# Kernel tuning notes

Measured on AMD Instinct MI355X. Metric: run time of the kernel, lower is better.

Reference implementation:

```python
import jax, jax.numpy as jnp
import numpy as np

B, S, D = 1, 2048, 1024   # batch, seq, hidden_size
I = 2048                  # intermediate_size (mlp1 emits 2*I, SwiGLU halves)
E = 8                     # num_experts
K = 2                     # experts_per_token
LIMIT = 7.0               # swiglu_limit
ALPHA = 1.702             # gpt-oss swiglu alpha
EPS = 1e-5                # RMSNorm eps


def setup_inputs() -> dict:
    key = jax.random.key(0)
    ks = jax.random.split(key, 4)
    s = 0.02
    return {
        "x": jax.random.normal(ks[0], (B, S, D), jnp.float32),
        "norm_scale": jnp.ones((D,), jnp.float32),
        "gate_w": jax.random.normal(ks[1], (D, E), jnp.float32) * s,
        "gate_b": jnp.zeros((E,), jnp.float32),
        "mlp1_w": jax.random.normal(ks[2], (E, D, 2 * I), jnp.float32) * s,
        "mlp1_b": jnp.zeros((E, 2 * I), jnp.float32),
        "mlp2_w": jax.random.normal(ks[3], (E, I, D), jnp.float32) * s,
        "mlp2_b": jnp.zeros((E, D), jnp.float32),
    }


def _swiglu(h):
    # gpt-oss interleaved SwiGLU with clamp limit
    x_glu = jnp.minimum(h[..., ::2], LIMIT)
    x_lin = jnp.clip(h[..., 1::2], -LIMIT, LIMIT)
    return x_glu * jax.nn.sigmoid(ALPHA * x_glu) * (x_lin + 1.0)


def _moe(t, gate_w, gate_b, mlp1_w, mlp1_b, mlp2_w, mlp2_b):
    T = t.shape[0]
    logits = t @ gate_w + gate_b                 # [T, E]
    top_v, top_i = jax.lax.top_k(logits, K)      # [T, K]
    probs = jax.nn.softmax(top_v, axis=-1)       # softmax over selected experts
    # dense routing-weight matrix, zero for unselected experts
    w = jnp.zeros((T, E), t.dtype).at[jnp.arange(T)[:, None], top_i].set(probs)

    def body(acc, ew):
        w1, b1, w2, b2, we = ew                  # per-expert params + weights [T]
        h = _swiglu(t @ w1 + b1)                 # [T, I]
        y = h @ w2 + b2                          # [T, D]
        return acc + we[:, None] * y, None

    acc0 = jnp.zeros((T, t.shape[1]), t.dtype)
    acc, _ = jax.lax.scan(body, acc0, (mlp1_w, mlp1_b, mlp2_w, mlp2_b, w.T))
    return acc


def reference(x, norm_scale, gate_w, gate_b, mlp1_w, mlp1_b, mlp2_w, mlp2_b):
    Bx, Sx, Dx = x.shape
    ms = jnp.mean(x * x, axis=-1, keepdims=True)
    t = (x * jax.lax.rsqrt(ms + EPS) * norm_scale).reshape(Bx * Sx, Dx)
    y = _moe(t, gate_w, gate_b, mlp1_w, mlp1_b, mlp2_w, mlp2_b)
    return x + y.reshape(Bx, Sx, Dx)
```

## Files before the change

### kernel.cpp

```cpp
#include <hip/hip_runtime.h>

typedef unsigned short u16;
typedef __attribute__((ext_vector_type(4))) unsigned short u16x4;
typedef __attribute__((ext_vector_type(8))) unsigned short u16x8;
typedef __attribute__((ext_vector_type(8))) short bf16x8;
typedef __attribute__((ext_vector_type(4))) float f32x4;

#define DEV static __device__ __forceinline__

DEV float bf2f(u16 b){ union{unsigned u; float f;} c; c.u = ((unsigned)b) << 16; return c.f; }
DEV u16 f2bf(float f){ union{float f; unsigned u;} c; c.f = f; unsigned u = c.u; u += 0x7FFF + ((u >> 16) & 1); return (u16)(u >> 16); }

DEV void gload16(const void* g, void* l){
  __builtin_amdgcn_global_load_lds((const __attribute__((address_space(1))) unsigned int*)g,
                                   (__attribute__((address_space(3))) unsigned int*)l, 16, 0, 0);
}

__global__ __launch_bounds__(256) void k_rms(
    const float* __restrict__ x, const float* __restrict__ nsc,
    const float* __restrict__ gw, const float* __restrict__ gb,
    u16* __restrict__ t, int* __restrict__ topi, float* __restrict__ topp)
{
  const int token = blockIdx.x, tid = threadIdx.x;
  const int wv = tid >> 6, lane = tid & 63;
  const float4 xv = *(const float4*)&x[(size_t)token * 1024 + tid * 4];
  float f[4] = {xv.x, xv.y, xv.z, xv.w};
  float ss = f[0]*f[0] + f[1]*f[1] + f[2]*f[2] + f[3]*f[3];
  #pragma unroll
  for (int o = 32; o > 0; o >>= 1) ss += __shfl_down(ss, o, 64);
  __shared__ float red[4];
  __shared__ float s_rs;
  if (lane == 0) red[wv] = ss;
  __syncthreads();
  if (tid == 0) s_rs = rsqrtf((red[0] + red[1] + red[2] + red[3]) * (1.0f / 1024.0f) + 1e-5f);
  __syncthreads();
  const float rs = s_rs;
  const float4 sv = *(const float4*)&nsc[tid * 4];
  const float sc[4] = {sv.x, sv.y, sv.z, sv.w};
  float tf[4]; u16x4 tv;
  #pragma unroll
  for (int j = 0; j < 4; ++j){ tf[j] = f[j] * rs * sc[j]; tv[j] = f2bf(tf[j]); }
  *(u16x4*)&t[(size_t)token * 1024 + tid * 4] = tv;

  float la[8] = {0,0,0,0,0,0,0,0};
  #pragma unroll
  for (int j = 0; j < 4; ++j){
    const int k = tid * 4 + j;
    const float4 g0 = *(const float4*)&gw[k * 8];
    const float4 g1 = *(const float4*)&gw[k * 8 + 4];
    la[0] += tf[j] * g0.x; la[1] += tf[j] * g0.y; la[2] += tf[j] * g0.z; la[3] += tf[j] * g0.w;
    la[4] += tf[j] * g1.x; la[5] += tf[j] * g1.y; la[6] += tf[j] * g1.z; la[7] += tf[j] * g1.w;
  }
  #pragma unroll
  for (int o = 32; o > 0; o >>= 1)
    #pragma unroll
    for (int e = 0; e < 8; ++e) la[e] += __shfl_down(la[e], o, 64);
  __shared__ float lred[4][8];
  if (lane == 0){
    #pragma unroll
    for (int e = 0; e < 8; ++e) lred[wv][e] = la[e];
  }
  __syncthreads();
  if (tid == 0){
    float lg[8];
    #pragma unroll
    for (int e = 0; e < 8; ++e) lg[e] = lred[0][e] + lred[1][e] + lred[2][e] + lred[3][e] + gb[e];
    int i0 = 0;
    for (int e = 1; e < 8; ++e) if (lg[e] > lg[i0]) i0 = e;
    int i1 = -1;
    for (int e = 0; e < 8; ++e) if (e != i0 && (i1 < 0 || lg[e] > lg[i1])) i1 = e;
    const float d = __expf(lg[i1] - lg[i0]);
    const float p0 = 1.0f / (1.0f + d);
    topi[token * 2] = i0; topi[token * 2 + 1] = i1;
    topp[token * 2] = p0; topp[token * 2 + 1] = d * p0;
  }
}

__global__ __launch_bounds__(256) void k_route(
    const int* __restrict__ topi, const float* __restrict__ topp,
    int* __restrict__ cnt, int* __restrict__ offs, int* __restrict__ tok_of,
    float* __restrict__ wt_of, int* __restrict__ slot_of, int* __restrict__ posg)
{
  __shared__ int c[8];
  __shared__ int o[8];
  const int tid = threadIdx.x;
  if (tid < 8) c[tid] = 0;
  __syncthreads();
  for (int a = tid; a < 4096; a += 256){
    int e = topi[a];
    posg[a] = atomicAdd(&c[e], 1);
  }
  __syncthreads();
  if (tid == 0){
    int run = 0;
    for (int e = 0; e < 8; ++e){ o[e] = run; offs[e] = run; cnt[e] = c[e]; run += c[e]; }
  }
  __syncthreads();
  for (int a = tid; a < 4096; a += 256){
    int e = topi[a];
    int s = o[e] + posg[a];
    tok_of[s] = a >> 1;
    wt_of[s] = topp[a];
    slot_of[a] = s;
  }
}

__global__ __launch_bounds__(256) void k_tr(const float* __restrict__ in, u16* __restrict__ outp, int R, int C)
{
  __shared__ __attribute__((aligned(16))) u16 tile[64][72];
  const size_t base = (size_t)blockIdx.z * (size_t)R * (size_t)C;
  const float* src = in + base;
  u16* dst = outp + base;
  const int r0 = blockIdx.y * 64, c0 = blockIdx.x * 64;
  const int tid = threadIdx.x;
  const int lr = tid >> 4;
  const int lc = (tid & 15) * 4;
  #pragma unroll
  for (int i = 0; i < 4; ++i){
    const float4 v = *(const float4*)&src[(size_t)(r0 + lr + i * 16) * C + c0 + lc];
    u16x4 b; b[0] = f2bf(v.x); b[1] = f2bf(v.y); b[2] = f2bf(v.z); b[3] = f2bf(v.w);
    *(u16x4*)&tile[lr + i * 16][lc] = b;
  }
  __syncthreads();
  const int lr2 = tid >> 3;
  const int lc2 = (tid & 7) * 8;
  #pragma unroll
  for (int i = 0; i < 2; ++i){
    const int cc = lr2 + i * 32;
    u16x8 v;
    #pragma unroll
    for (int j = 0; j < 8; ++j) v[j] = tile[lc2 + j][cc];
    *(u16x8*)&dst[(size_t)(c0 + cc) * R + r0 + lc2] = v;
  }
}

__global__ __launch_bounds__(256) void k_gemm1(
    const u16* __restrict__ t, const u16* __restrict__ w1t, const float* __restrict__ b1,
    const int* __restrict__ cnt, const int* __restrict__ offs, const int* __restrict__ tok_of,
    u16* __restrict__ h)
{
  const int e = blockIdx.z;
  const int count = cnt[e];
  const int m0 = blockIdx.y * 128;
  if (m0 >= count) return;
  const int off = offs[e];
  const int n0 = blockIdx.x * 128;

  __shared__ __attribute__((aligned(16))) u16 As[128 * 32];
  __shared__ __attribute__((aligned(16))) u16 Bs[128 * 32];

  const int tid = threadIdx.x, wv = tid >> 6, lane = tid & 63;
  const int srow = wv * 32 + (lane >> 2);
  const int kc = (lane & 3) * 8;

  const u16* aptr[2]; const u16* bptr[2];
  #pragma unroll
  for (int i = 0; i < 2; ++i){
    int r = m0 + srow + i * 16; if (r > count - 1) r = count - 1;
    const int tok = tok_of[off + r];
    aptr[i] = t + (size_t)tok * 1024 + kc;
    bptr[i] = w1t + ((size_t)e * 4096 + n0 + srow + i * 16) * 1024 + kc;
  }
  u16* lA0 = &As[(wv * 32) * 32];      u16* lA1 = &As[(wv * 32 + 16) * 32];
  u16* lB0 = &Bs[(wv * 32) * 32];      u16* lB1 = &Bs[(wv * 32 + 16) * 32];

  const int wm = wv & 1, wn = wv >> 1;
  const int fr = lane & 15, q8 = (lane >> 4) * 8;

  f32x4 acc[4][4];
  #pragma unroll
  for (int a = 0; a < 4; ++a)
    #pragma unroll
    for (int b = 0; b < 4; ++b) acc[a][b] = (f32x4){0.f, 0.f, 0.f, 0.f};

  for (int k0 = 0; k0 < 1024; k0 += 32){
    gload16(aptr[0], lA0); gload16(aptr[1], lA1);
    gload16(bptr[0], lB0); gload16(bptr[1], lB1);
    aptr[0] += 32; aptr[1] += 32; bptr[0] += 32; bptr[1] += 32;
    __syncthreads();
    bf16x8 af[4], bq[4];
    #pragma unroll
    for (int fm = 0; fm < 4; ++fm) af[fm] = *(const bf16x8*)&As[(wm * 64 + fm * 16 + fr) * 32 + q8];
    #pragma unroll
    for (int fn = 0; fn < 4; ++fn) bq[fn] = *(const bf16x8*)&Bs[(wn * 64 + fn * 16 + fr) * 32 + q8];
    #pragma unroll
    for (int fm = 0; fm < 4; ++fm)
      #pragma unroll
      for (int fn = 0; fn < 4; ++fn)
        acc[fm][fn] = __builtin_amdgcn_mfma_f32_16x16x32_bf16(af[fm], bq[fn], acc[fm][fn], 0, 0, 0);
    __syncthreads();
  }

  const int cb = n0 + wn * 64 + fr;
  float b1v[4];
  #pragma unroll
  for (int fn = 0; fn < 4; ++fn) b1v[fn] = b1[e * 4096 + cb + fn * 16];
  const int rq = (lane >> 4) * 4;
  const bool ev = ((lane & 1) == 0);
  #pragma unroll
  for (int fm = 0; fm < 4; ++fm)
    #pragma unroll
    for (int fn = 0; fn < 4; ++fn)
      #pragma unroll
      for (int r = 0; r < 4; ++r){
        const float val = acc[fm][fn][r] + b1v[fn];
        const float oth = __shfl_xor(val, 1, 64);
        if (ev){
          const int row = m0 + wm * 64 + fm * 16 + rq + r;
          if (row < count){
            const float g = fminf(val, 7.0f);
            const float l = fminf(fmaxf(oth, -7.0f), 7.0f);
            const float o = g / (1.0f + __expf(-1.702f * g)) * (l + 1.0f);
            h[(size_t)(off + row) * 2048 + ((cb + fn * 16) >> 1)] = f2bf(o);
          }
        }
      }
}

__global__ __launch_bounds__(256) void k_gemm2(
    const u16* __restrict__ h, const u16* __restrict__ w2t, const float* __restrict__ b2,
    const int* __restrict__ cnt, const int* __restrict__ offs, const float* __restrict__ wt_of,
    u16* __restrict__ ys)
{
  const int e = blockIdx.z;
  const int count = cnt[e];
  const int m0 = blockIdx.y * 64;
  if (m0 >= count) return;
  const int off = offs[e];
  const int n0 = blockIdx.x * 64;

  __shared__ __attribute__((aligned(16))) u16 As[64 * 32];
  __shared__ __attribute__((aligned(16))) u16 Bs[64 * 32];

  const int tid = threadIdx.x, wv = tid >> 6, lane = tid & 63;
  const int srow = wv * 16 + (lane >> 2);
  const int kc = (lane & 3) * 8;
  int r = m0 + srow; if (r > count - 1) r = count - 1;
  const u16* aptr = h + (size_t)(off + r) * 2048 + kc;
  const u16* bptr = w2t + ((size_t)e * 1024 + n0 + srow) * 2048 + kc;
  u16* lA = &As[(wv * 16) * 32];
  u16* lB = &Bs[(wv * 16) * 32];

  const int wm = wv & 1, wn = wv >> 1;
  const int fr = lane & 15, q8 = (lane >> 4) * 8;

  f32x4 acc[2][2];
  #pragma unroll
  for (int a = 0; a < 2; ++a)
    #pragma unroll
    for (int b = 0; b < 2; ++b) acc[a][b] = (f32x4){0.f, 0.f, 0.f, 0.f};

  for (int k0 = 0; k0 < 2048; k0 += 32){
    gload16(aptr, lA); gload16(bptr, lB);
    aptr += 32; bptr += 32;
    __syncthreads();
    bf16x8 af[2], bq[2];
    #pragma unroll
    for (int fm = 0; fm < 2; ++fm) af[fm] = *(const bf16x8*)&As[(wm * 32 + fm * 16 + fr) * 32 + q8];
    #pragma unroll
    for (int fn = 0; fn < 2; ++fn) bq[fn] = *(const bf16x8*)&Bs[(wn * 32 + fn * 16 + fr) * 32 + q8];
    #pragma unroll
    for (int fm = 0; fm < 2; ++fm)
      #pragma unroll
      for (int fn = 0; fn < 2; ++fn)
        acc[fm][fn] = __builtin_amdgcn_mfma_f32_16x16x32_bf16(af[fm], bq[fn], acc[fm][fn], 0, 0, 0);
    __syncthreads();
  }

  const int cb = n0 + wn * 32 + fr;
  float b2v[2];
  #pragma unroll
  for (int fn = 0; fn < 2; ++fn) b2v[fn] = b2[e * 1024 + cb + fn * 16];
  const int rq = (lane >> 4) * 4;
  #pragma unroll
  for (int fm = 0; fm < 2; ++fm)
    #pragma unroll
    for (int rr = 0; rr < 4; ++rr){
      const int row = m0 + wm * 32 + fm * 16 + rq + rr;
      if (row < count){
        const float wt = wt_of[off + row];
        #pragma unroll
        for (int fn = 0; fn < 2; ++fn){
          const float v = (acc[fm][fn][rr] + b2v[fn]) * wt;
          ys[(size_t)(off + row) * 1024 + cb + fn * 16] = f2bf(v);
        }
      }
    }
}

__global__ __launch_bounds__(256) void k_final(
    const float* __restrict__ x, const u16* __restrict__ ys,
    const int* __restrict__ slot_of, float* __restrict__ out)
{
  const int gid = blockIdx.x * 256 + threadIdx.x;
  const int token = gid >> 8;
  const int c0 = (gid & 255) * 4;
  const int s0 = slot_of[token * 2], s1 = slot_of[token * 2 + 1];
  const float4 xv = *(const float4*)&x[(size_t)token * 1024 + c0];
  const u16x4 y0 = *(const u16x4*)&ys[(size_t)s0 * 1024 + c0];
  const u16x4 y1 = *(const u16x4*)&ys[(size_t)s1 * 1024 + c0];
  float4 o;
  o.x = xv.x + bf2f(y0[0]) + bf2f(y1[0]);
  o.y = xv.y + bf2f(y0[1]) + bf2f(y1[1]);
  o.z = xv.z + bf2f(y0[2]) + bf2f(y1[2]);
  o.w = xv.w + bf2f(y0[3]) + bf2f(y1[3]);
  *(float4*)&out[(size_t)token * 1024 + c0] = o;
}

extern "C" void kernel_launch(void* const* d_in, const int* in_sizes, int n_in,
                              void* d_out, int out_size, void* d_ws, size_t ws_size,
                              hipStream_t stream)
{
  const float* x   = (const float*)d_in[0];
  const float* nsc = (const float*)d_in[1];
  const float* gw  = (const float*)d_in[2];
  const float* gb  = (const float*)d_in[3];
  const float* w1  = (const float*)d_in[4];
  const float* b1  = (const float*)d_in[5];
  const float* w2  = (const float*)d_in[6];
  const float* b2  = (const float*)d_in[7];
  float* out = (float*)d_out;
  char* ws = (char*)d_ws;

  size_t o = 0;
  auto alloc = [&](size_t bytes){ size_t r = o; o = (o + bytes + 255) & ~(size_t)255; return r; };
  const size_t o_t    = alloc((size_t)2048 * 1024 * 2);
  const size_t o_w1t  = alloc((size_t)8 * 4096 * 1024 * 2);
  const size_t o_w2t  = alloc((size_t)8 * 1024 * 2048 * 2);
  const size_t o_h    = alloc((size_t)4096 * 2048 * 2);
  const size_t o_ys   = alloc((size_t)4096 * 1024 * 2);
  const size_t o_topi = alloc(4096 * 4);
  const size_t o_topp = alloc(4096 * 4);
  const size_t o_posg = alloc(4096 * 4);
  const size_t o_tok  = alloc(4096 * 4);
  const size_t o_wt   = alloc(4096 * 4);
  const size_t o_slot = alloc(4096 * 4);
  const size_t o_cnt  = alloc(8 * 4);
  const size_t o_offs = alloc(8 * 4);
  if (ws_size < o) return;

  u16*   t_ws  = (u16*)(ws + o_t);
  u16*   w1t   = (u16*)(ws + o_w1t);
  u16*   w2t   = (u16*)(ws + o_w2t);
  u16*   h_ws  = (u16*)(ws + o_h);
  u16*   ys    = (u16*)(ws + o_ys);
  int*   topi  = (int*)(ws + o_topi);
  float* topp  = (float*)(ws + o_topp);
  int*   posg  = (int*)(ws + o_posg);
  int*   tok   = (int*)(ws + o_tok);
  float* wt    = (float*)(ws + o_wt);
  int*   slot  = (int*)(ws + o_slot);
  int*   cnt   = (int*)(ws + o_cnt);
  int*   offs  = (int*)(ws + o_offs);

  k_rms  <<<2048, 256, 0, stream>>>(x, nsc, gw, gb, t_ws, topi, topp);
  k_route<<<1, 256, 0, stream>>>(topi, topp, cnt, offs, tok, wt, slot, posg);
  k_tr   <<<dim3(64, 16, 8), 256, 0, stream>>>(w1, w1t, 1024, 4096);
  k_tr   <<<dim3(16, 32, 8), 256, 0, stream>>>(w2, w2t, 2048, 1024);
  k_gemm1<<<dim3(32, 16, 8), 256, 0, stream>>>(t_ws, w1t, b1, cnt, offs, tok, h_ws);
  k_gemm2<<<dim3(16, 32, 8), 256, 0, stream>>>(h_ws, w2t, b2, cnt, offs, wt, ys);
  k_final<<<2048, 256, 0, stream>>>(x, ys, slot, out);
}
```

Baseline: 419.4 us.

## Double K-tile depth with XOR-swizzled LDS and enlarge GEMM2 M tile

```diff
diff --git a/kernel.cpp b/kernel.cpp
--- a/kernel.cpp
+++ b/kernel.cpp
@@ -146,26 +146,27 @@
   const int off = offs[e];
   const int n0 = blockIdx.x * 128;
 
-  __shared__ __attribute__((aligned(16))) u16 As[128 * 32];
-  __shared__ __attribute__((aligned(16))) u16 Bs[128 * 32];
+  __shared__ __attribute__((aligned(16))) u16 As[128 * 64];
+  __shared__ __attribute__((aligned(16))) u16 Bs[128 * 64];
 
   const int tid = threadIdx.x, wv = tid >> 6, lane = tid & 63;
-  const int srow = wv * 32 + (lane >> 2);
-  const int kc = (lane & 3) * 8;
-
-  const u16* aptr[2]; const u16* bptr[2];
-  #pragma unroll
-  for (int i = 0; i < 2; ++i){
-    int r = m0 + srow + i * 16; if (r > count - 1) r = count - 1;
-    const int tok = tok_of[off + r];
-    aptr[i] = t + (size_t)tok * 1024 + kc;
-    bptr[i] = w1t + ((size_t)e * 4096 + n0 + srow + i * 16) * 1024 + kc;
-  }
-  u16* lA0 = &As[(wv * 32) * 32];      u16* lA1 = &As[(wv * 32 + 16) * 32];
-  u16* lB0 = &Bs[(wv * 32) * 32];      u16* lB1 = &Bs[(wv * 32 + 16) * 32];
+  const int arl = lane >> 3;
+  const int axu = (lane & 7) ^ arl;
+
+  const u16* asrc[4]; const u16* bsrc[4];
+  u16 *adst[4], *bdst[4];
+  #pragma unroll
+  for (int i = 0; i < 4; ++i){
+    const int rr = i * 32 + wv * 8 + arl;
+    int r = m0 + rr; if (r > count - 1) r = count - 1;
+    asrc[i] = t + (size_t)tok_of[off + r] * 1024 + axu * 8;
+    bsrc[i] = w1t + ((size_t)e * 4096 + n0 + rr) * 1024 + axu * 8;
+    adst[i] = &As[(i * 32 + wv * 8) * 64];
+    bdst[i] = &Bs[(i * 32 + wv * 8) * 64];
+  }
 
   const int wm = wv & 1, wn = wv >> 1;
-  const int fr = lane & 15, q8 = (lane >> 4) * 8;
+  const int fr = lane & 15, q = lane >> 4;
 
   f32x4 acc[4][4];
   #pragma unroll
@@ -173,21 +174,26 @@
     #pragma unroll
     for (int b = 0; b < 4; ++b) acc[a][b] = (f32x4){0.f, 0.f, 0.f, 0.f};
 
-  for (int k0 = 0; k0 < 1024; k0 += 32){
-    gload16(aptr[0], lA0); gload16(aptr[1], lA1);
-    gload16(bptr[0], lB0); gload16(bptr[1], lB1);
-    aptr[0] += 32; aptr[1] += 32; bptr[0] += 32; bptr[1] += 32;
+  for (int k0 = 0; k0 < 1024; k0 += 64){
+    #pragma unroll
+    for (int i = 0; i < 4; ++i){ gload16(asrc[i], adst[i]); asrc[i] += 64; }
+    #pragma unroll
+    for (int i = 0; i < 4; ++i){ gload16(bsrc[i], bdst[i]); bsrc[i] += 64; }
     __syncthreads();
-    bf16x8 af[4], bq[4];
-    #pragma unroll
-    for (int fm = 0; fm < 4; ++fm) af[fm] = *(const bf16x8*)&As[(wm * 64 + fm * 16 + fr) * 32 + q8];
-    #pragma unroll
-    for (int fn = 0; fn < 4; ++fn) bq[fn] = *(const bf16x8*)&Bs[(wn * 64 + fn * 16 + fr) * 32 + q8];
-    #pragma unroll
-    for (int fm = 0; fm < 4; ++fm)
-      #pragma unroll
-      for (int fn = 0; fn < 4; ++fn)
-        acc[fm][fn] = __builtin_amdgcn_mfma_f32_16x16x32_bf16(af[fm], bq[fn], acc[fm][fn], 0, 0, 0);
+    #pragma unroll
+    for (int hh = 0; hh < 2; ++hh){
+      const int pu = (((hh * 4) + q) ^ (fr & 7)) * 8;
+      bf16x8 af[4], bq[4];
+      #pragma unroll
+      for (int fm = 0; fm < 4; ++fm) af[fm] = *(const bf16x8*)&As[(wm * 64 + fm * 16 + fr) * 64 + pu];
+      #pragma unroll
+      for (int fn = 0; fn < 4; ++fn) bq[fn] = *(const bf16x8*)&Bs[(wn * 64 + fn * 16 + fr) * 64 + pu];
+      #pragma unroll
+      for (int fm = 0; fm < 4; ++fm)
+        #pragma unroll
+        for (int fn = 0; fn < 4; ++fn)
+          acc[fm][fn] = __builtin_amdgcn_mfma_f32_16x16x32_bf16(af[fm], bq[fn], acc[fm][fn], 0, 0, 0);
+    }
     __syncthreads();
   }
 
@@ -195,7 +201,7 @@
   float b1v[4];
   #pragma unroll
   for (int fn = 0; fn < 4; ++fn) b1v[fn] = b1[e * 4096 + cb + fn * 16];
-  const int rq = (lane >> 4) * 4;
+  const int rq = q * 4;
   const bool ev = ((lane & 1) == 0);
   #pragma unroll
   for (int fm = 0; fm < 4; ++fm)
@@ -224,46 +230,63 @@
 {
   const int e = blockIdx.z;
   const int count = cnt[e];
-  const int m0 = blockIdx.y * 64;
+  const int m0 = blockIdx.y * 128;
   if (m0 >= count) return;
   const int off = offs[e];
   const int n0 = blockIdx.x * 64;
 
-  __shared__ __attribute__((aligned(16))) u16 As[64 * 32];
-  __shared__ __attribute__((aligned(16))) u16 Bs[64 * 32];
+  __shared__ __attribute__((aligned(16))) u16 As[128 * 64];
+  __shared__ __attribute__((aligned(16))) u16 Bs[64 * 64];
 
   const int tid = threadIdx.x, wv = tid >> 6, lane = tid & 63;
-  const int srow = wv * 16 + (lane >> 2);
-  const int kc = (lane & 3) * 8;
-  int r = m0 + srow; if (r > count - 1) r = count - 1;
-  const u16* aptr = h + (size_t)(off + r) * 2048 + kc;
-  const u16* bptr = w2t + ((size_t)e * 1024 + n0 + srow) * 2048 + kc;
-  u16* lA = &As[(wv * 16) * 32];
-  u16* lB = &Bs[(wv * 16) * 32];
+  const int arl = lane >> 3;
+  const int axu = (lane & 7) ^ arl;
+
+  const u16* asrc[4]; const u16* bsrc[2];
+  u16 *adst[4], *bdst[2];
+  #pragma unroll
+  for (int i = 0; i < 4; ++i){
+    const int rr = i * 32 + wv * 8 + arl;
+    int r = m0 + rr; if (r > count - 1) r = count - 1;
+    asrc[i] = h + (size_t)(off + r) * 2048 + axu * 8;
+    adst[i] = &As[(i * 32 + wv * 8) * 64];
+  }
+  #pragma unroll
+  for (int i = 0; i < 2; ++i){
+    const int rr = i * 32 + wv * 8 + arl;
+    bsrc[i] = w2t + ((size_t)e * 1024 + n0 + rr) * 2048 + axu * 8;
+    bdst[i] = &Bs[(i * 32 + wv * 8) * 64];
+  }
 
   const int wm = wv & 1, wn = wv >> 1;
-  const int fr = lane & 15, q8 = (lane >> 4) * 8;
-
-  f32x4 acc[2][2];
-  #pragma unroll
-  for (int a = 0; a < 2; ++a)
+  const int fr = lane & 15, q = lane >> 4;
+
+  f32x4 acc[4][2];
+  #pragma unroll
+  for (int a = 0; a < 4; ++a)
     #pragma unroll
     for (int b = 0; b < 2; ++b) acc[a][b] = (f32x4){0.f, 0.f, 0.f, 0.f};
 
-  for (int k0 = 0; k0 < 2048; k0 += 32){
-    gload16(aptr, lA); gload16(bptr, lB);
-    aptr += 32; bptr += 32;
+  for (int k0 = 0; k0 < 2048; k0 += 64){
+    #pragma unroll
+    for (int i = 0; i < 4; ++i){ gload16(asrc[i], adst[i]); asrc[i] += 64; }
+    #pragma unroll
+    for (int i = 0; i < 2; ++i){ gload16(bsrc[i], bdst[i]); bsrc[i] += 64; }
     __syncthreads();
-    bf16x8 af[2], bq[2];
-    #pragma unroll
-    for (int fm = 0; fm < 2; ++fm) af[fm] = *(const bf16x8*)&As[(wm * 32 + fm * 16 + fr) * 32 + q8];
-    #pragma unroll
-    for (int fn = 0; fn < 2; ++fn) bq[fn] = *(const bf16x8*)&Bs[(wn * 32 + fn * 16 + fr) * 32 + q8];
-    #pragma unroll
-    for (int fm = 0; fm < 2; ++fm)
-      #pragma unroll
-      for (int fn = 0; fn < 2; ++fn)
-        acc[fm][fn] = __builtin_amdgcn_mfma_f32_16x16x32_bf16(af[fm], bq[fn], acc[fm][fn], 0, 0, 0);
+    #pragma unroll
+    for (int hh = 0; hh < 2; ++hh){
+      const int pu = (((hh * 4) + q) ^ (fr & 7)) * 8;
+      bf16x8 af[4], bq[2];
+      #pragma unroll
+      for (int fm = 0; fm < 4; ++fm) af[fm] = *(const bf16x8*)&As[(wm * 64 + fm * 16 + fr) * 64 + pu];
+      #pragma unroll
+      for (int fn = 0; fn < 2; ++fn) bq[fn] = *(const bf16x8*)&Bs[(wn * 32 + fn * 16 + fr) * 64 + pu];
+      #pragma unroll
+      for (int fm = 0; fm < 4; ++fm)
+        #pragma unroll
+        for (int fn = 0; fn < 2; ++fn)
+          acc[fm][fn] = __builtin_amdgcn_mfma_f32_16x16x32_bf16(af[fm], bq[fn], acc[fm][fn], 0, 0, 0);
+    }
     __syncthreads();
   }
 
@@ -271,12 +294,12 @@
   float b2v[2];
   #pragma unroll
   for (int fn = 0; fn < 2; ++fn) b2v[fn] = b2[e * 1024 + cb + fn * 16];
-  const int rq = (lane >> 4) * 4;
-  #pragma unroll
-  for (int fm = 0; fm < 2; ++fm)
+  const int rq = q * 4;
+  #pragma unroll
+  for (int fm = 0; fm < 4; ++fm)
     #pragma unroll
     for (int rr = 0; rr < 4; ++rr){
-      const int row = m0 + wm * 32 + fm * 16 + rq + rr;
+      const int row = m0 + wm * 64 + fm * 16 + rq + rr;
       if (row < count){
         const float wt = wt_of[off + row];
         #pragma unroll
```

Result: no change. 411.4 us (-1.9%).
